# Kernel tuning notes

Measured on AMD Instinct MI355X. Metric: run time of the kernel, lower is better.

## Reference

```python
import jax, jax.numpy as jnp
import numpy as np

MIN_VAL = -100000.0
K = 48          # num_tags
START = 46      # tag_to_ix['<START>']
END = 47        # tag_to_ix['<END>']
B = 512         # batch of sentences (vmapped; original code is per-sentence)
T = 1024        # sentence length


def setup_inputs() -> dict:
    key = jax.random.key(0)
    k1, k2, k3 = jax.random.split(key, 3)
    feats = jax.random.normal(k1, (B, T, K), dtype=jnp.float32)
    trans = jax.random.normal(k2, (K, K), dtype=jnp.float32) * 0.1
    # structural constraints from CRF.__init__: nothing transitions FROM END
    # (column END) and nothing transitions TO START (row START)
    trans = trans.at[START, :].set(MIN_VAL).at[:, END].set(MIN_VAL)
    tags = jax.random.randint(k3, (B, T), 0, START)  # gold tags, never START/END
    return {"feats": feats, "trans": trans, "tags": tags}


def _neg_ll_single(feats, trans, tags):
    # feats: [T, K], trans: [K, K] (trans[i, j] = score of j -> i), tags: [T]
    init_alpha = jnp.full((K,), MIN_VAL, dtype=feats.dtype).at[START].set(0.0)

    def step(alpha, feat):
        # alpha_new[i] = logsumexp_j(trans[i, j] + alpha[j]) + feat[i]
        alpha = jax.nn.logsumexp(trans + alpha[None, :], axis=1) + feat
        return alpha, None

    alpha, _ = jax.lax.scan(step, init_alpha, feats)
    log_z = jax.nn.logsumexp(alpha + trans[END])  # forward_alg

    # get_gold_scores: sum_i trans[tags[i+1], tags[i]] + feat[i][tags[i+1]]
    prev = jnp.concatenate([jnp.array([START], dtype=tags.dtype), tags[:-1]])
    emit = jnp.take_along_axis(feats, tags[:, None], axis=1)[:, 0]  # [T]
    gold = jnp.sum(trans[tags, prev] + emit) + trans[END, tags[-1]]

    return log_z - gold  # neg_ll_loss


def reference(feats, trans, tags):
    # per-sentence negative log-likelihood, shape [B]
    return jax.vmap(_neg_ll_single, in_axes=(0, None, 0))(feats, trans, tags)
```

## Files before the change

kernel.cpp:

```cpp
#include <hip/hip_runtime.h>
#include <math.h>

#define KK 48
#define TT 1024
#define BB 512
#define START_TAG 46
#define END_TAG 47
#define NSEG 16
#define OWN (TT / NSEG)
#define WARM 16
#define DEPTH 8
#define SLOTB 3072
#define NGRP (BB / 16)
#define NPAIR (NGRP * NSEG)
#define WSF 50

typedef _Float16 h2 __attribute__((ext_vector_type(2)));
typedef _Float16 f16x4 __attribute__((ext_vector_type(4)));
typedef float f32x4 __attribute__((ext_vector_type(4)));

#if defined(__HIP_DEVICE_COMPILE__)
  #if __has_builtin(__builtin_amdgcn_mfma_f32_16x16x16f16)
    #define MFMA16(A, B, C) __builtin_amdgcn_mfma_f32_16x16x16f16((A), (B), (C), 0, 0, 0)
  #elif __has_builtin(__builtin_amdgcn_mfma_f32_16x16x16_f16)
    #define MFMA16(A, B, C) __builtin_amdgcn_mfma_f32_16x16x16_f16((A), (B), (C), 0, 0, 0)
  #else
    #error "no 16x16x16 f16 mfma on this target"
  #endif
  #define SB() __builtin_amdgcn_sched_barrier(0)
  __device__ __forceinline__ void gld16(const float* g, char* l) {
      __builtin_amdgcn_global_load_lds(
          (const __attribute__((address_space(1))) void*)g,
          (__attribute__((address_space(3))) void*)l, 16, 0, 0);
  }
  #define WAITV(n) asm volatile("s_waitcnt vmcnt(" #n ")" ::: "memory")
#else
  #define MFMA16(A, B, C) (C)
  #define SB()
  __device__ __forceinline__ void gld16(const float*, char*) {}
  #define WAITV(n)
#endif

__device__ __forceinline__ h2 pkrtz(float a, float b) {
    return __builtin_bit_cast(h2, __builtin_amdgcn_cvt_pkrtz(a, b));
}


template <bool EXACT>
__device__ __forceinline__ void run_seg(const float* __restrict__ fbl,
                                        const float* __restrict__ trans,
                                        char* ldsb,
                                        int lane, int g4, int r0, int nsteps,
                                        float (&wv)[3][4], int& esumO, int& eswmO,
                                        float& q0O) {
    f16x4 Af[3][3];
    #pragma unroll
    for (int m = 0; m < 3; ++m) {
        const int row = 16 * m + (lane & 15);
        #pragma unroll
        for (int c = 0; c < 3; ++c) {
            #pragma unroll
            for (int j = 0; j < 4; ++j)
                Af[m][c][j] = (_Float16)__expf(trans[row * KK + 16 * c + 4 * g4 + j]);
        }
    }

    f16x4 bf[3];
    if (EXACT) {
        #pragma unroll
        for (int c = 0; c < 3; ++c) bf[c] = (f16x4)(_Float16)0.0f;
        if (g4 == 3) bf[2][2] = (_Float16)1.0f;
    } else {
        #pragma unroll
        for (int c = 0; c < 3; ++c) bf[c] = (f16x4)(_Float16)1.0f;
    }

    int esum = 0, eswm = 0;
    float q0v = 1.0f;

    WAITV(0);
    SB();
    #pragma unroll
    for (int j = 0; j < DEPTH; ++j) {
        int t = r0 + j; if (t > TT - 1) t = TT - 1;
        char* slot = ldsb + j * SLOTB;
        #pragma unroll
        for (int c = 0; c < 3; ++c)
            gld16(fbl + (size_t)t * KK + 16 * c + 4 * g4, slot + c * 1024);
    }

    for (int s0 = 0; s0 < nsteps; s0 += DEPTH) {
        #pragma unroll
        for (int j = 0; j < DEPTH; ++j) {
            const int st = s0 + j;
            char* slot = ldsb + j * SLOTB;
            WAITV(21);
            SB();
            f32x4 ftc[3];
            #pragma unroll
            for (int c = 0; c < 3; ++c)
                ftc[c] = *(const f32x4*)(slot + c * 1024 + lane * 16);
            float ef[3][4];
            #pragma unroll
            for (int m = 0; m < 3; ++m)
                #pragma unroll
                for (int r = 0; r < 4; ++r) ef[m][r] = __expf(ftc[m][r]);
            SB();
            {
                int tn = r0 + st + DEPTH; if (tn > TT - 1) tn = TT - 1;
                #pragma unroll
                for (int c = 0; c < 3; ++c)
                    gld16(fbl + (size_t)tn * KK + 16 * c + 4 * g4, slot + c * 1024);
            }
            const f32x4 z = {0.f, 0.f, 0.f, 0.f};
            f32x4 a0 = MFMA16(Af[0][0], bf[0], z);
            f32x4 a1 = MFMA16(Af[1][0], bf[0], z);
            f32x4 a2 = MFMA16(Af[2][0], bf[0], z);
            a0 = MFMA16(Af[0][1], bf[1], a0);
            a1 = MFMA16(Af[1][1], bf[1], a1);
            a2 = MFMA16(Af[2][1], bf[1], a2);
            a0 = MFMA16(Af[0][2], bf[2], a0);
            a1 = MFMA16(Af[1][2], bf[2], a1);
            a2 = MFMA16(Af[2][2], bf[2], a2);
            #pragma unroll
            for (int r = 0; r < 4; ++r) {
                wv[0][r] = a0[r] * ef[0][r];
                wv[1][r] = a1[r] * ef[1][r];
                wv[2][r] = a2[r] * ef[2][r];
            }
            float ref = __shfl(wv[0][0], lane & 15, 64);
            int eb = ((__float_as_int(ref) >> 23) & 0xff) - 127;
            esum += eb;
            float sc = __int_as_float((127 - eb) << 23);
            #pragma unroll
            for (int m = 0; m < 3; ++m)
                #pragma unroll
                for (int r = 0; r < 4; ++r) wv[m][r] *= sc;
            if (!EXACT && st == WARM - 1) { eswm = esum; q0v = ref * sc; }
            #pragma unroll
            for (int m = 0; m < 3; ++m) {
                h2 lo = pkrtz(wv[m][0], wv[m][1]);
                h2 hi = pkrtz(wv[m][2], wv[m][3]);
                bf[m][0] = lo.x; bf[m][1] = lo.y; bf[m][2] = hi.x; bf[m][3] = hi.y;
            }
        }
    }
    esumO = esum; eswmO = eswm; q0O = q0v;
}

__global__ __launch_bounds__(64)
void crf_seg_kernel(const float* __restrict__ feats,
                    const float* __restrict__ trans,
                    float* __restrict__ ws) {
    const int pair = blockIdx.x;
    const int g = pair >> 4;
    const int seg = pair & 15;
    const int lane = threadIdx.x & 63;
    const int g4 = lane >> 4;
    const float* fbl = feats + (size_t)(g * 16 + (lane & 15)) * TT * KK;

    __shared__ __align__(16) char ldsb[DEPTH * SLOTB];

    float wv[3][4];
    int esum, eswm; float q0v;
    if (seg == 0) run_seg<true >(fbl, trans, ldsb, lane, g4, 0, OWN,
                                 wv, esum, eswm, q0v);
    else          run_seg<false>(fbl, trans, ldsb, lane, g4, seg * OWN - WARM,
                                 OWN + WARM, wv, esum, eswm, q0v);

    float* base = ws + ((size_t)pair * 16 + (lane & 15)) * WSF;
    #pragma unroll
    for (int m = 0; m < 3; ++m)
        #pragma unroll
        for (int r = 0; r < 4; ++r)
            base[16 * m + 4 * g4 + r] = wv[m][r];
    if (lane < 16) {
        float* b2 = ws + ((size_t)pair * 16 + lane) * WSF;
        b2[48] = (float)(esum - eswm);
        b2[49] = q0v;
    }
}

__global__ __launch_bounds__(256)
void crf_combine(const float* __restrict__ feats,
                 const float* __restrict__ trans,
                 const int* __restrict__ tags,
                 const float* __restrict__ ws,
                 float* __restrict__ out) {
    const int s = blockIdx.x;
    const int g = s >> 4;
    const int sidx = s & 15;
    const int tid = threadIdx.x;
    const int lane = tid & 63;
    const int w = tid >> 6;
    const int* tg = tags + (size_t)s * TT;
    const float* fbs = feats + (size_t)s * TT * KK;

    __shared__ float red[4];

    float gacc = 0.0f;
    #pragma unroll
    for (int it = 0; it < TT / 256; ++it) {
        int t = tid + it * 256;
        int cur = tg[t];
        int prev = (t == 0) ? START_TAG : tg[t - 1];
        gacc += trans[cur * KK + prev] + fbs[(size_t)t * KK + cur];
    }
    #pragma unroll
    for (int off = 32; off; off >>= 1) gacc += __shfl_xor(gacc, off, 64);
    if (lane == 0) red[w] = gacc;
    __syncthreads();

    if (w == 0) {
        float val = 0.0f;
        if (lane < KK)
            val = __expf(trans[END_TAG * KK + lane]) *
                  ws[(((size_t)g * 16 + 15) * 16 + sidx) * WSF + lane];
        #pragma unroll
        for (int off = 32; off; off >>= 1) val += __shfl_xor(val, off, 64);

        float stv = 0.0f;
        if (lane >= 1 && lane < NSEG) {
            float Uprev0 = ws[(((size_t)g * 16 + lane - 1) * 16 + sidx) * WSF + 0];
            float q0w    = ws[(((size_t)g * 16 + lane) * 16 + sidx) * WSF + 49];
            stv = __logf(Uprev0) - __logf(q0w);
        }
        if (lane < NSEG)
            stv += ws[(((size_t)g * 16 + lane) * 16 + sidx) * WSF + 48] *
                   0.6931471805599453f;
        #pragma unroll
        for (int off = 32; off; off >>= 1) stv += __shfl_xor(stv, off, 64);

        if (lane == 0) {
            float gold = red[0] + red[1] + red[2] + red[3] +
                         trans[END_TAG * KK + tg[TT - 1]];
            out[s] = __logf(val) + stv - gold;
        }
    }
}

extern "C" void kernel_launch(void* const* d_in, const int* in_sizes, int n_in,
                              void* d_out, int out_size, void* d_ws, size_t ws_size,
                              hipStream_t stream) {
    const float* feats = (const float*)d_in[0];
    const float* trans = (const float*)d_in[1];
    const int* tags = (const int*)d_in[2];
    float* out = (float*)d_out;
    float* ws = (float*)d_ws;

    crf_seg_kernel<<<NPAIR, 64, 0, stream>>>(feats, trans, ws);
    crf_combine<<<BB, 256, 0, stream>>>(feats, trans, tags, ws, out);
}
```

Before: 171.6 us.

## Stage feature rows in contiguous 8-step chunks with double-buffered LDS

Replaces the per-timestep 3-load ring (one 16-byte load per lane per column block, scattered across 16 sentences) with bulk chunk staging. Each chunk copies 8 consecutive timesteps for all 16 sentences into LDS using 25 load instructions whose lanes walk contiguous global memory. LDS rows are padded to a stride of 1584 bytes, and chunks are double-buffered so the next chunk loads while the current 8 steps compute. The aim is better coalescing and fewer wait points in the serial recurrence. The cost is more LDS, an lgkmcnt wait per chunk, and reliance on the remainder masking for the 99-wide padded layout.

```diff
diff --git a/kernel.cpp b/kernel.cpp
--- a/kernel.cpp
+++ b/kernel.cpp
@@ -9,8 +9,10 @@
 #define NSEG 16
 #define OWN (TT / NSEG)
 #define WARM 16
-#define DEPTH 8
-#define SLOTB 3072
+#define CH 8
+#define SSTRIDE 1584
+#define NINST 25
+#define CHB (NINST * 1024)
 #define NGRP (BB / 16)
 #define NPAIR (NGRP * NSEG)
 #define WSF 50
@@ -34,11 +36,13 @@
           (__attribute__((address_space(3))) void*)l, 16, 0, 0);
   }
   #define WAITV(n) asm volatile("s_waitcnt vmcnt(" #n ")" ::: "memory")
+  #define WAITL()  asm volatile("s_waitcnt lgkmcnt(0)" ::: "memory")
 #else
   #define MFMA16(A, B, C) (C)
   #define SB()
   __device__ __forceinline__ void gld16(const float*, char*) {}
   #define WAITV(n)
+  #define WAITL()
 #endif
 
 __device__ __forceinline__ h2 pkrtz(float a, float b) {
@@ -46,17 +50,39 @@
 }
 
 
+__device__ __forceinline__ void stage_chunk(const float* __restrict__ gbase,
+                                            char* buf, const int (&off)[NINST],
+                                            int br) {
+    const int rowoff = br * KK;
+    #pragma unroll
+    for (int i = 0; i < NINST; ++i)
+        gld16(gbase + off[i] + rowoff, buf + i * 1024);
+}
+
 template <bool EXACT>
-__device__ __forceinline__ void run_seg(const float* __restrict__ fbl,
+__device__ __forceinline__ void run_seg(const float* __restrict__ gbase,
                                         const float* __restrict__ trans,
-                                        char* ldsb,
-                                        int lane, int g4, int r0, int nsteps,
+                                        char* lds,
+                                        int lane, int r0, int nsteps,
                                         float (&wv)[3][4], int& esumO, int& eswmO,
                                         float& q0O) {
+    const int s = lane & 15;
+    const int g4 = lane >> 4;
+
+    int off[NINST];
+    #pragma unroll
+    for (int i = 0; i < NINST; ++i) {
+        int u = i * 64 + lane;
+        int q = (u * 663) >> 16;
+        int rem16 = u - q * 99;
+        bool valid = (q < 16) & (rem16 < 96);
+        off[i] = valid ? (q * (TT * KK) + rem16 * 4) : 0;
+    }
+
     f16x4 Af[3][3];
     #pragma unroll
     for (int m = 0; m < 3; ++m) {
-        const int row = 16 * m + (lane & 15);
+        const int row = 16 * m + s;
         #pragma unroll
         for (int c = 0; c < 3; ++c) {
             #pragma unroll
@@ -78,40 +104,27 @@
     int esum = 0, eswm = 0;
     float q0v = 1.0f;
 
-    WAITV(0);
-    SB();
-    #pragma unroll
-    for (int j = 0; j < DEPTH; ++j) {
-        int t = r0 + j; if (t > TT - 1) t = TT - 1;
-        char* slot = ldsb + j * SLOTB;
-        #pragma unroll
-        for (int c = 0; c < 3; ++c)
-            gld16(fbl + (size_t)t * KK + 16 * c + 4 * g4, slot + c * 1024);
-    }
-
-    for (int s0 = 0; s0 < nsteps; s0 += DEPTH) {
-        #pragma unroll
-        for (int j = 0; j < DEPTH; ++j) {
-            const int st = s0 + j;
-            char* slot = ldsb + j * SLOTB;
-            WAITV(21);
-            SB();
+    const int nch = nsteps / CH;
+    stage_chunk(gbase, lds, off, r0);
+    stage_chunk(gbase, lds + CHB, off, r0 + CH);
+
+    for (int ch = 0; ch < nch; ++ch) {
+        char* buf = lds + (ch & 1) * CHB;
+        WAITV(25);
+        SB();
+        #pragma unroll
+        for (int st2 = 0; st2 < CH; ++st2) {
+            const int st = ch * CH + st2;
+            const char* p = buf + s * SSTRIDE + st2 * 192 + g4 * 16;
             f32x4 ftc[3];
             #pragma unroll
             for (int c = 0; c < 3; ++c)
-                ftc[c] = *(const f32x4*)(slot + c * 1024 + lane * 16);
+                ftc[c] = *(const f32x4*)(p + c * 64);
             float ef[3][4];
             #pragma unroll
             for (int m = 0; m < 3; ++m)
                 #pragma unroll
                 for (int r = 0; r < 4; ++r) ef[m][r] = __expf(ftc[m][r]);
-            SB();
-            {
-                int tn = r0 + st + DEPTH; if (tn > TT - 1) tn = TT - 1;
-                #pragma unroll
-                for (int c = 0; c < 3; ++c)
-                    gld16(fbl + (size_t)tn * KK + 16 * c + 4 * g4, slot + c * 1024);
-            }
             const f32x4 z = {0.f, 0.f, 0.f, 0.f};
             f32x4 a0 = MFMA16(Af[0][0], bf[0], z);
             f32x4 a1 = MFMA16(Af[1][0], bf[0], z);
@@ -128,7 +141,7 @@
                 wv[1][r] = a1[r] * ef[1][r];
                 wv[2][r] = a2[r] * ef[2][r];
             }
-            float ref = __shfl(wv[0][0], lane & 15, 64);
+            float ref = __shfl(wv[0][0], s, 64);
             int eb = ((__float_as_int(ref) >> 23) & 0xff) - 127;
             esum += eb;
             float sc = __int_as_float((127 - eb) << 23);
@@ -144,6 +157,10 @@
                 bf[m][0] = lo.x; bf[m][1] = lo.y; bf[m][2] = hi.x; bf[m][3] = hi.y;
             }
         }
+        WAITL();
+        int brn = r0 + (ch + 2) * CH;
+        if (brn > TT - CH) brn = TT - CH;
+        stage_chunk(gbase, buf, off, brn);
     }
     esumO = esum; eswmO = eswm; q0O = q0v;
 }
@@ -157,15 +174,15 @@
     const int seg = pair & 15;
     const int lane = threadIdx.x & 63;
     const int g4 = lane >> 4;
-    const float* fbl = feats + (size_t)(g * 16 + (lane & 15)) * TT * KK;
-
-    __shared__ __align__(16) char ldsb[DEPTH * SLOTB];
+    const float* gbase = feats + (size_t)g * 16 * TT * KK;
+
+    __shared__ __align__(16) char lds[2 * CHB];
 
     float wv[3][4];
     int esum, eswm; float q0v;
-    if (seg == 0) run_seg<true >(fbl, trans, ldsb, lane, g4, 0, OWN,
+    if (seg == 0) run_seg<true >(gbase, trans, lds, lane, 0, OWN,
                                  wv, esum, eswm, q0v);
-    else          run_seg<false>(fbl, trans, ldsb, lane, g4, seg * OWN - WARM,
+    else          run_seg<false>(gbase, trans, lds, lane, seg * OWN - WARM,
                                  OWN + WARM, wv, esum, eswm, q0v);
 
     float* base = ws + ((size_t)pair * 16 + (lane & 15)) * WSF;
```

Measured after the change: 168.6 us. Within noise of the previous version (-1.8%).
